# Kernel optimization log

Hardware: AMD Instinct MI355X
Metric: run time of the kernel (lower is better)

Reference implementation:

```python
import jax, jax.numpy as jnp
import numpy as np

HIDDEN = 2048
INTER = 8192
COMPRESSION = 128.9

def _n_ctrl(out_size, in_size):
    return max(16, int(out_size * in_size / COMPRESSION))

def _catmull_rom_grid(n_ctrl, n_samples):
    # static (numpy, float64) sampling grid over [0, n_ctrl-1] to avoid fp32 precision loss
    t = np.linspace(0.0, n_ctrl - 1.0, n_samples, dtype=np.float64)
    i = np.clip(np.floor(t).astype(np.int64), 0, n_ctrl - 2)
    f = (t - i).astype(np.float32)
    idx = np.stack([np.clip(i + k, 0, n_ctrl - 1) for k in (-1, 0, 1, 2)], axis=0)  # [4, N]
    return jnp.asarray(idx.astype(np.int32)), jnp.asarray(f)

def spline_reconstruct(control_points, out_size, in_size):
    """Cubic (Catmull-Rom, order-3) interpolation of 1D control points to a dense [out,in] weight."""
    n = out_size * in_size
    idx, f = _catmull_rom_grid(control_points.shape[0], n)
    p0, p1, p2, p3 = control_points[idx[0]], control_points[idx[1]], control_points[idx[2]], control_points[idx[3]]
    f2 = f * f
    f3 = f2 * f
    w = 0.5 * (2.0 * p1 + (p2 - p0) * f
               + (2.0 * p0 - 5.0 * p1 + 4.0 * p2 - p3) * f2
               + (3.0 * p1 - p0 - 3.0 * p2 + p3) * f3)
    return w.reshape(out_size, in_size)

def setup_inputs() -> dict:
    key = jax.random.key(0)
    k0, k1, k2, k3 = jax.random.split(key, 4)
    hidden_states = jax.random.normal(k0, (4, 2048, HIDDEN), dtype=jnp.float32)
    gate_cp = jax.random.normal(k1, (_n_ctrl(INTER, HIDDEN),), dtype=jnp.float32) * 0.02
    up_cp = jax.random.normal(k2, (_n_ctrl(INTER, HIDDEN),), dtype=jnp.float32) * 0.02
    down_cp = jax.random.normal(k3, (_n_ctrl(HIDDEN, INTER),), dtype=jnp.float32) * 0.02
    return {"hidden_states": hidden_states, "gate_cp": gate_cp, "up_cp": up_cp, "down_cp": down_cp}

def reference(hidden_states, gate_cp, up_cp, down_cp):
    gate_w = spline_reconstruct(gate_cp, INTER, HIDDEN)   # [I, H]
    up_w = spline_reconstruct(up_cp, INTER, HIDDEN)       # [I, H]
    down_w = spline_reconstruct(down_cp, HIDDEN, INTER)   # [H, I]
    gate = jnp.einsum('bsh,ih->bsi', hidden_states, gate_w)
    up = jnp.einsum('bsh,ih->bsi', hidden_states, up_w)
    inter = jax.nn.silu(gate) * up
    return jnp.einsum('bsi,hi->bsh', inter, down_w)
```

## Files before the change

kernel.cpp:

```cpp
#include <hip/hip_runtime.h>
#include <hip/hip_bf16.h>
#include <math.h>

using bf16 = __hip_bfloat16;
typedef __bf16 bf16x8 __attribute__((ext_vector_type(8)));
typedef float  f32x4  __attribute__((ext_vector_type(4)));

#define BK 64

__global__ void spline_recon8_kernel(const float* __restrict__ cp,
                                     bf16* __restrict__ w,
                                     int n8, int n_ctrl, double step) {
    int k8 = blockIdx.x * blockDim.x + threadIdx.x;
    if (k8 >= n8) return;
    long long kbase = (long long)k8 * 8;
    bf16x8 o;
#pragma unroll
    for (int u = 0; u < 8; ++u) {
        double t = (double)(kbase + u) * step;
        int i = (int)t;
        if (i > n_ctrl - 2) i = n_ctrl - 2;
        float f = (float)(t - (double)i);
        float p0 = cp[i > 0 ? i - 1 : 0];
        float p1 = cp[i];
        float p2 = cp[i + 1];
        float p3 = cp[(i + 2) <= (n_ctrl - 1) ? (i + 2) : (n_ctrl - 1)];
        float f2 = f * f;
        float f3 = f2 * f;
        float v = 0.5f * (2.0f * p1
                          + (p2 - p0) * f
                          + (2.0f * p0 - 5.0f * p1 + 4.0f * p2 - p3) * f2
                          + (3.0f * p1 - p0 - 3.0f * p2 + p3) * f3);
        o[u] = (__bf16)v;
    }
    *reinterpret_cast<bf16x8*>(w + kbase) = o;
}

__global__ void cvt_f32_bf16_8_kernel(const float4* __restrict__ x,
                                      bf16* __restrict__ y, int n8) {
    int k = blockIdx.x * blockDim.x + threadIdx.x;
    if (k >= n8) return;
    float4 a = x[2 * k];
    float4 b = x[2 * k + 1];
    bf16x8 o;
    o[0] = (__bf16)a.x; o[1] = (__bf16)a.y; o[2] = (__bf16)a.z; o[3] = (__bf16)a.w;
    o[4] = (__bf16)b.x; o[5] = (__bf16)b.y; o[6] = (__bf16)b.z; o[7] = (__bf16)b.w;
    *reinterpret_cast<bf16x8*>(y + (long long)k * 8) = o;
}

__device__ __forceinline__ void async_load16(const bf16* g, bf16* l) {
    __builtin_amdgcn_global_load_lds(
        (const __attribute__((address_space(1))) void*)g,
        (__attribute__((address_space(3))) void*)l,
        16, 0, 0);
}

__global__ __launch_bounds__(512, 4) void fused_gate_up_kernel(
    const bf16* __restrict__ A,
    const bf16* __restrict__ Bg,
    const bf16* __restrict__ Bu,
    bf16* __restrict__ C,
    int M, int N, int K) {
    __shared__ __align__(16) bf16 smem[3 * 128 * BK];
    bf16* As  = smem;
    bf16* Bgs = smem + 128 * BK;
    bf16* Bus = smem + 2 * 128 * BK;

    const int tid  = threadIdx.x;
    const int lane = tid & 63;
    const int wave = tid >> 6;
    const int wq   = wave & 3;
    const int wm   = (wq >> 1) * 64;
    const int wn   = (wq & 1) * 64;
    const bool is_gate = wave < 4;

    const long long brow = (long long)blockIdx.y * 128;
    const long long bcol = (long long)blockIdx.x * 128;

    const int srow = tid >> 3;
    const int skb  = ((tid & 7) ^ (srow & 7)) * 8;
    const bf16* ga0 = A  + (brow + srow) * (long long)K + skb;
    const bf16* ga1 = A  + (brow + srow + 64) * (long long)K + skb;
    const bf16* gg0 = Bg + (bcol + srow) * (long long)K + skb;
    const bf16* gg1 = Bg + (bcol + srow + 64) * (long long)K + skb;
    const bf16* gu0 = Bu + (bcol + srow) * (long long)K + skb;
    const bf16* gu1 = Bu + (bcol + srow + 64) * (long long)K + skb;
    bf16* la0 = As  + tid * 8;
    bf16* la1 = As  + 4096 + tid * 8;
    bf16* lg0 = Bgs + tid * 8;
    bf16* lg1 = Bgs + 4096 + tid * 8;
    bf16* lu0 = Bus + tid * 8;
    bf16* lu1 = Bus + 4096 + tid * 8;

    const bf16* Bsel = is_gate ? Bgs : Bus;
    const int fm = wm + (lane & 15);
    const int fn = wn + (lane & 15);
    const int qk = lane >> 4;

    f32x4 acc[4][4] = {};

    for (int k0 = 0; k0 < K; k0 += BK) {
        async_load16(ga0, la0); ga0 += BK;
        async_load16(ga1, la1); ga1 += BK;
        async_load16(gg0, lg0); gg0 += BK;
        async_load16(gg1, lg1); gg1 += BK;
        async_load16(gu0, lu0); gu0 += BK;
        async_load16(gu1, lu1); gu1 += BK;
        __syncthreads();

#pragma unroll
        for (int h = 0; h < 2; ++h) {
            bf16x8 afr[4], bfr[4];
            const int hc = (h << 2) | qk;
            const int ccA = (hc ^ (fm & 7)) * 8;
            const int ccB = (hc ^ (fn & 7)) * 8;
#pragma unroll
            for (int i = 0; i < 4; ++i)
                afr[i] = *reinterpret_cast<const bf16x8*>(
                    &As[(fm + i * 16) * BK + ccA]);
#pragma unroll
            for (int j = 0; j < 4; ++j)
                bfr[j] = *reinterpret_cast<const bf16x8*>(
                    &Bsel[(fn + j * 16) * BK + ccB]);
#pragma unroll
            for (int i = 0; i < 4; ++i)
#pragma unroll
                for (int j = 0; j < 4; ++j)
                    acc[i][j] = __builtin_amdgcn_mfma_f32_16x16x32_bf16(
                        afr[i], bfr[j], acc[i][j], 0, 0, 0);
        }
        __syncthreads();
    }

    bf16* Epi = smem;
    if (is_gate) {
#pragma unroll
        for (int i = 0; i < 4; ++i)
#pragma unroll
            for (int j = 0; j < 4; ++j)
#pragma unroll
                for (int r = 0; r < 4; ++r) {
                    int row = wm + i * 16 + (lane >> 4) * 4 + r;
                    int col = wn + j * 16 + (lane & 15);
                    float v = acc[i][j][r];
                    float s = v / (1.0f + expf(-v));
                    Epi[row * 128 + col] = __float2bfloat16(s);
                }
    }
    __syncthreads();
    if (!is_gate) {
#pragma unroll
        for (int i = 0; i < 4; ++i)
#pragma unroll
            for (int j = 0; j < 4; ++j)
#pragma unroll
                for (int r = 0; r < 4; ++r) {
                    int row = wm + i * 16 + (lane >> 4) * 4 + r;
                    int col = wn + j * 16 + (lane & 15);
                    float s = __bfloat162float(Epi[row * 128 + col]);
                    float v = s * acc[i][j][r];
                    C[(brow + row) * (long long)N + bcol + col] = __float2bfloat16(v);
                }
    }
}

__global__ __launch_bounds__(512, 4) void gemm_down2_kernel(
    const bf16* __restrict__ A,
    const bf16* __restrict__ B,
    float* __restrict__ C,
    int M, int N, int K) {
    __shared__ __align__(16) bf16 As[128 * BK];
    __shared__ __align__(16) bf16 Bs[256 * BK];

    const int tid  = threadIdx.x;
    const int lane = tid & 63;
    const int wave = tid >> 6;
    const int half = wave >> 2;
    const int wq   = wave & 3;
    const int wm   = (wq >> 1) * 64;
    const int wn   = half * 128 + (wq & 1) * 64;

    const long long brow = (long long)blockIdx.y * 128;
    const long long bcol = (long long)blockIdx.x * 256;

    const int srow = tid >> 3;
    const int skb  = ((tid & 7) ^ (srow & 7)) * 8;
    const bf16* ga0 = A + (brow + srow) * (long long)K + skb;
    const bf16* ga1 = A + (brow + srow + 64) * (long long)K + skb;
    const bf16* gb0 = B + (bcol + srow) * (long long)K + skb;
    const bf16* gb1 = B + (bcol + srow + 64) * (long long)K + skb;
    const bf16* gb2 = B + (bcol + srow + 128) * (long long)K + skb;
    const bf16* gb3 = B + (bcol + srow + 192) * (long long)K + skb;
    bf16* la0 = As + tid * 8;
    bf16* la1 = As + 4096 + tid * 8;
    bf16* lb0 = Bs + tid * 8;
    bf16* lb1 = Bs + 4096 + tid * 8;
    bf16* lb2 = Bs + 8192 + tid * 8;
    bf16* lb3 = Bs + 12288 + tid * 8;

    const int fm = wm + (lane & 15);
    const int fn = wn + (lane & 15);
    const int qk = lane >> 4;

    f32x4 acc[4][4] = {};

    for (int k0 = 0; k0 < K; k0 += BK) {
        async_load16(ga0, la0); ga0 += BK;
        async_load16(ga1, la1); ga1 += BK;
        async_load16(gb0, lb0); gb0 += BK;
        async_load16(gb1, lb1); gb1 += BK;
        async_load16(gb2, lb2); gb2 += BK;
        async_load16(gb3, lb3); gb3 += BK;
        __syncthreads();

#pragma unroll
        for (int h = 0; h < 2; ++h) {
            bf16x8 afr[4], bfr[4];
            const int hc = (h << 2) | qk;
            const int ccA = (hc ^ (fm & 7)) * 8;
            const int ccB = (hc ^ (fn & 7)) * 8;
#pragma unroll
            for (int i = 0; i < 4; ++i)
                afr[i] = *reinterpret_cast<const bf16x8*>(
                    &As[(fm + i * 16) * BK + ccA]);
#pragma unroll
            for (int j = 0; j < 4; ++j)
                bfr[j] = *reinterpret_cast<const bf16x8*>(
                    &Bs[(fn + j * 16) * BK + ccB]);
#pragma unroll
            for (int i = 0; i < 4; ++i)
#pragma unroll
                for (int j = 0; j < 4; ++j)
                    acc[i][j] = __builtin_amdgcn_mfma_f32_16x16x32_bf16(
                        afr[i], bfr[j], acc[i][j], 0, 0, 0);
        }
        __syncthreads();
    }

#pragma unroll
    for (int i = 0; i < 4; ++i)
#pragma unroll
        for (int j = 0; j < 4; ++j)
#pragma unroll
            for (int r = 0; r < 4; ++r) {
                long long row = brow + wm + i * 16 + (lane >> 4) * 4 + r;
                long long col = bcol + wn + j * 16 + (lane & 15);
                C[row * N + col] = acc[i][j][r];
            }
}

extern "C" void kernel_launch(void* const* d_in, const int* in_sizes, int n_in,
                              void* d_out, int out_size, void* d_ws, size_t ws_size,
                              hipStream_t stream) {
    const float* hs  = (const float*)d_in[0];
    const float* gcp = (const float*)d_in[1];
    const float* ucp = (const float*)d_in[2];
    const float* dcp = (const float*)d_in[3];

    const int M = 8192;
    const int H = 2048;
    const int I = 8192;
    const int NW = H * I;
    const int n_ctrl_g = in_sizes[1];
    const int n_ctrl_u = in_sizes[2];
    const int n_ctrl_d = in_sizes[3];

    bf16* Xb    = (bf16*)d_ws;
    bf16* Wg    = Xb + (size_t)M * H;
    bf16* Wu    = Wg + (size_t)NW;
    bf16* Wd    = Wu + (size_t)NW;
    bf16* inter = Wd + (size_t)NW;

    const int nX8 = (M * H) / 8;
    cvt_f32_bf16_8_kernel<<<(nX8 + 255) / 256, 256, 0, stream>>>(
        (const float4*)hs, Xb, nX8);

    double step_g = (double)(n_ctrl_g - 1) / (double)(NW - 1);
    double step_u = (double)(n_ctrl_u - 1) / (double)(NW - 1);
    double step_d = (double)(n_ctrl_d - 1) / (double)(NW - 1);
    const int n8 = NW / 8;
    spline_recon8_kernel<<<(n8 + 255) / 256, 256, 0, stream>>>(gcp, Wg, n8, n_ctrl_g, step_g);
    spline_recon8_kernel<<<(n8 + 255) / 256, 256, 0, stream>>>(ucp, Wu, n8, n_ctrl_u, step_u);
    spline_recon8_kernel<<<(n8 + 255) / 256, 256, 0, stream>>>(dcp, Wd, n8, n_ctrl_d, step_d);

    fused_gate_up_kernel<<<dim3(I / 128, M / 128), 512, 0, stream>>>(
        Xb, Wg, Wu, inter, M, I, H);

    gemm_down2_kernel<<<dim3(H / 256, M / 128), 512, 0, stream>>>(
        inter, Wd, (float*)d_out, M, H, I);
}
```

Baseline: 922.6 us.

## Halve block threads and double per-wave MFMA tile in both GEMMs

Both GEMM kernels drop from 512 to 256 threads per block, and each wave now computes a 64x128 output tile (4x8 MFMA accumulators) instead of 64x64. Block tile sizes stay the same, so each thread issues more async loads per K step and each loaded A fragment is reused across twice as many MFMAs. This aims to raise fragment reuse and cut LDS read traffic per MFMA. The cost is doubled accumulator registers, which limits occupancy (launch bounds lowered to 256,2), and fewer waves are left to hide latency.

```diff
diff --git a/kernel.cpp b/kernel.cpp
--- a/kernel.cpp
+++ b/kernel.cpp
@@ -55,7 +55,7 @@
         16, 0, 0);
 }
 
-__global__ __launch_bounds__(512, 4) void fused_gate_up_kernel(
+__global__ __launch_bounds__(256, 2) void fused_gate_up_kernel(
     const bf16* __restrict__ A,
     const bf16* __restrict__ Bg,
     const bf16* __restrict__ Bu,
@@ -63,69 +63,62 @@
     int M, int N, int K) {
     __shared__ __align__(16) bf16 smem[3 * 128 * BK];
     bf16* As  = smem;
-    bf16* Bgs = smem + 128 * BK;
-    bf16* Bus = smem + 2 * 128 * BK;
+    bf16* Bgs = smem + 8192;
+    bf16* Bus = smem + 16384;
 
     const int tid  = threadIdx.x;
     const int lane = tid & 63;
     const int wave = tid >> 6;
-    const int wq   = wave & 3;
-    const int wm   = (wq >> 1) * 64;
-    const int wn   = (wq & 1) * 64;
-    const bool is_gate = wave < 4;
+    const int wm   = (wave & 1) * 64;
+    const bool is_gate = wave < 2;
 
     const long long brow = (long long)blockIdx.y * 128;
     const long long bcol = (long long)blockIdx.x * 128;
 
     const int srow = tid >> 3;
     const int skb  = ((tid & 7) ^ (srow & 7)) * 8;
-    const bf16* ga0 = A  + (brow + srow) * (long long)K + skb;
-    const bf16* ga1 = A  + (brow + srow + 64) * (long long)K + skb;
-    const bf16* gg0 = Bg + (bcol + srow) * (long long)K + skb;
-    const bf16* gg1 = Bg + (bcol + srow + 64) * (long long)K + skb;
-    const bf16* gu0 = Bu + (bcol + srow) * (long long)K + skb;
-    const bf16* gu1 = Bu + (bcol + srow + 64) * (long long)K + skb;
-    bf16* la0 = As  + tid * 8;
-    bf16* la1 = As  + 4096 + tid * 8;
-    bf16* lg0 = Bgs + tid * 8;
-    bf16* lg1 = Bgs + 4096 + tid * 8;
-    bf16* lu0 = Bus + tid * 8;
-    bf16* lu1 = Bus + 4096 + tid * 8;
+    const bf16* ga = A  + (brow + srow) * (long long)K + skb;
+    const bf16* gg = Bg + (bcol + srow) * (long long)K + skb;
+    const bf16* gu = Bu + (bcol + srow) * (long long)K + skb;
+    const long long rstep = 32LL * K;
 
     const bf16* Bsel = is_gate ? Bgs : Bus;
     const int fm = wm + (lane & 15);
-    const int fn = wn + (lane & 15);
+    const int fnb = lane & 15;
     const int qk = lane >> 4;
-
-    f32x4 acc[4][4] = {};
+    const int ccAbase = fm & 7;
+    const int ccBbase = fnb & 7;
+
+    f32x4 acc[4][8] = {};
 
     for (int k0 = 0; k0 < K; k0 += BK) {
-        async_load16(ga0, la0); ga0 += BK;
-        async_load16(ga1, la1); ga1 += BK;
-        async_load16(gg0, lg0); gg0 += BK;
-        async_load16(gg1, lg1); gg1 += BK;
-        async_load16(gu0, lu0); gu0 += BK;
-        async_load16(gu1, lu1); gu1 += BK;
+#pragma unroll
+        for (int r = 0; r < 4; ++r) {
+            async_load16(ga + r * rstep, As  + r * 2048 + tid * 8);
+            async_load16(gg + r * rstep, Bgs + r * 2048 + tid * 8);
+            async_load16(gu + r * rstep, Bus + r * 2048 + tid * 8);
+        }
+        ga += BK; gg += BK; gu += BK;
         __syncthreads();
 
 #pragma unroll
         for (int h = 0; h < 2; ++h) {
-            bf16x8 afr[4], bfr[4];
             const int hc = (h << 2) | qk;
-            const int ccA = (hc ^ (fm & 7)) * 8;
-            const int ccB = (hc ^ (fn & 7)) * 8;
+            const int ccA = (hc ^ ccAbase) * 8;
+            const int ccB = (hc ^ ccBbase) * 8;
+            bf16x8 afr[4], bfr[8];
 #pragma unroll
             for (int i = 0; i < 4; ++i)
                 afr[i] = *reinterpret_cast<const bf16x8*>(
                     &As[(fm + i * 16) * BK + ccA]);
 #pragma unroll
-            for (int j = 0; j < 4; ++j)
+            for (int j = 0; j < 8; ++j)
                 bfr[j] = *reinterpret_cast<const bf16x8*>(
-                    &Bsel[(fn + j * 16) * BK + ccB]);
-#pragma unroll
-            for (int i = 0; i < 4; ++i)
-#pragma unroll
-                for (int j = 0; j < 4; ++j)
+                    &Bsel[(fnb + j * 16) * BK + ccB]);
+#pragma unroll
+            for (int i = 0; i < 4; ++i)
+#pragma unroll
+                for (int j = 0; j < 8; ++j)
                     acc[i][j] = __builtin_amdgcn_mfma_f32_16x16x32_bf16(
                         afr[i], bfr[j], acc[i][j], 0, 0, 0);
         }
@@ -137,11 +130,11 @@
 #pragma unroll
         for (int i = 0; i < 4; ++i)
 #pragma unroll
-            for (int j = 0; j < 4; ++j)
+            for (int j = 0; j < 8; ++j)
 #pragma unroll
                 for (int r = 0; r < 4; ++r) {
-                    int row = wm + i * 16 + (lane >> 4) * 4 + r;
-                    int col = wn + j * 16 + (lane & 15);
+                    int row = wm + i * 16 + qk * 4 + r;
+                    int col = j * 16 + (lane & 15);
                     float v = acc[i][j][r];
                     float s = v / (1.0f + expf(-v));
                     Epi[row * 128 + col] = __float2bfloat16(s);
@@ -152,11 +145,11 @@
 #pragma unroll
         for (int i = 0; i < 4; ++i)
 #pragma unroll
-            for (int j = 0; j < 4; ++j)
+            for (int j = 0; j < 8; ++j)
 #pragma unroll
                 for (int r = 0; r < 4; ++r) {
-                    int row = wm + i * 16 + (lane >> 4) * 4 + r;
-                    int col = wn + j * 16 + (lane & 15);
+                    int row = wm + i * 16 + qk * 4 + r;
+                    int col = j * 16 + (lane & 15);
                     float s = __bfloat162float(Epi[row * 128 + col]);
                     float v = s * acc[i][j][r];
                     C[(brow + row) * (long long)N + bcol + col] = __float2bfloat16(v);
@@ -164,7 +157,7 @@
     }
 }
 
-__global__ __launch_bounds__(512, 4) void gemm_down2_kernel(
+__global__ __launch_bounds__(256, 2) void gemm_down2_kernel(
     const bf16* __restrict__ A,
     const bf16* __restrict__ B,
     float* __restrict__ C,
@@ -175,62 +168,54 @@
     const int tid  = threadIdx.x;
     const int lane = tid & 63;
     const int wave = tid >> 6;
-    const int half = wave >> 2;
-    const int wq   = wave & 3;
-    const int wm   = (wq >> 1) * 64;
-    const int wn   = half * 128 + (wq & 1) * 64;
+    const int wm   = (wave >> 1) * 64;
+    const int wn   = (wave & 1) * 128;
 
     const long long brow = (long long)blockIdx.y * 128;
     const long long bcol = (long long)blockIdx.x * 256;
 
     const int srow = tid >> 3;
     const int skb  = ((tid & 7) ^ (srow & 7)) * 8;
-    const bf16* ga0 = A + (brow + srow) * (long long)K + skb;
-    const bf16* ga1 = A + (brow + srow + 64) * (long long)K + skb;
-    const bf16* gb0 = B + (bcol + srow) * (long long)K + skb;
-    const bf16* gb1 = B + (bcol + srow + 64) * (long long)K + skb;
-    const bf16* gb2 = B + (bcol + srow + 128) * (long long)K + skb;
-    const bf16* gb3 = B + (bcol + srow + 192) * (long long)K + skb;
-    bf16* la0 = As + tid * 8;
-    bf16* la1 = As + 4096 + tid * 8;
-    bf16* lb0 = Bs + tid * 8;
-    bf16* lb1 = Bs + 4096 + tid * 8;
-    bf16* lb2 = Bs + 8192 + tid * 8;
-    bf16* lb3 = Bs + 12288 + tid * 8;
+    const bf16* ga = A + (brow + srow) * (long long)K + skb;
+    const bf16* gb = B + (bcol + srow) * (long long)K + skb;
+    const long long rstep = 32LL * K;
 
     const int fm = wm + (lane & 15);
-    const int fn = wn + (lane & 15);
+    const int fnb = wn + (lane & 15);
     const int qk = lane >> 4;
-
-    f32x4 acc[4][4] = {};
+    const int ccAbase = fm & 7;
+    const int ccBbase = fnb & 7;
+
+    f32x4 acc[4][8] = {};
 
     for (int k0 = 0; k0 < K; k0 += BK) {
-        async_load16(ga0, la0); ga0 += BK;
-        async_load16(ga1, la1); ga1 += BK;
-        async_load16(gb0, lb0); gb0 += BK;
-        async_load16(gb1, lb1); gb1 += BK;
-        async_load16(gb2, lb2); gb2 += BK;
-        async_load16(gb3, lb3); gb3 += BK;
+#pragma unroll
+        for (int r = 0; r < 4; ++r)
+            async_load16(ga + r * rstep, As + r * 2048 + tid * 8);
+#pragma unroll
+        for (int r = 0; r < 8; ++r)
+            async_load16(gb + r * rstep, Bs + r * 2048 + tid * 8);
+        ga += BK; gb += BK;
         __syncthreads();
 
 #pragma unroll
         for (int h = 0; h < 2; ++h) {
-            bf16x8 afr[4], bfr[4];
             const int hc = (h << 2) | qk;
-            const int ccA = (hc ^ (fm & 7)) * 8;
-            const int ccB = (hc ^ (fn & 7)) * 8;
+            const int ccA = (hc ^ ccAbase) * 8;
+            const int ccB = (hc ^ ccBbase) * 8;
+            bf16x8 afr[4], bfr[8];
 #pragma unroll
             for (int i = 0; i < 4; ++i)
                 afr[i] = *reinterpret_cast<const bf16x8*>(
                     &As[(fm + i * 16) * BK + ccA]);
 #pragma unroll
-            for (int j = 0; j < 4; ++j)
+            for (int j = 0; j < 8; ++j)
                 bfr[j] = *reinterpret_cast<const bf16x8*>(
-                    &Bs[(fn + j * 16) * BK + ccB]);
-#pragma unroll
-            for (int i = 0; i < 4; ++i)
-#pragma unroll
-                for (int j = 0; j < 4; ++j)
+                    &Bs[(fnb + j * 16) * BK + ccB]);
+#pragma unroll
+            for (int i = 0; i < 4; ++i)
+#pragma unroll
+                for (int j = 0; j < 8; ++j)
                     acc[i][j] = __builtin_amdgcn_mfma_f32_16x16x32_bf16(
                         afr[i], bfr[j], acc[i][j], 0, 0, 0);
         }
@@ -240,10 +225,10 @@
 #pragma unroll
     for (int i = 0; i < 4; ++i)
 #pragma unroll
-        for (int j = 0; j < 4; ++j)
+        for (int j = 0; j < 8; ++j)
 #pragma unroll
             for (int r = 0; r < 4; ++r) {
-                long long row = brow + wm + i * 16 + (lane >> 4) * 4 + r;
+                long long row = brow + wm + i * 16 + qk * 4 + r;
                 long long col = bcol + wn + j * 16 + (lane & 15);
                 C[row * N + col] = acc[i][j][r];
             }
@@ -283,9 +268,9 @@
     spline_recon8_kernel<<<(n8 + 255) / 256, 256, 0, stream>>>(ucp, Wu, n8, n_ctrl_u, step_u);
     spline_recon8_kernel<<<(n8 + 255) / 256, 256, 0, stream>>>(dcp, Wd, n8, n_ctrl_d, step_d);
 
-    fused_gate_up_kernel<<<dim3(I / 128, M / 128), 512, 0, stream>>>(
+    fused_gate_up_kernel<<<dim3(I / 128, M / 128), 256, 0, stream>>>(
         Xb, Wg, Wu, inter, M, I, H);
 
-    gemm_down2_kernel<<<dim3(H / 256, M / 128), 512, 0, stream>>>(
+    gemm_down2_kernel<<<dim3(H / 256, M / 128), 256, 0, stream>>>(
         inter, Wd, (float*)d_out, M, H, I);
 }
```

Result: no change. 925.5 us (+0.3%).
